# Optimization experiments

Measured on AMD Instinct MI355X. Metric: run time of the kernel, lower is better.

## Reference

```python
import jax, jax.numpy as jnp
import numpy as np
from jax.scipy.special import digamma, gammaln

B, N, H, W, D = 16, 1024, 32, 32, 256
TEMP = 0.5
KL_WEIGHT = 1e-3


def setup_inputs() -> dict:
    key = jax.random.key(0)
    k1, k2, k3 = jax.random.split(key, 3)
    logits = jax.random.normal(k1, (B, N, H, W), dtype=jnp.float32)
    # codebook initialized uniform(-1/N, 1/N) as in init_type == 'uniform'
    codebook = jax.random.uniform(k2, (N, D), dtype=jnp.float32,
                                  minval=-1.0 / N, maxval=1.0 / N)
    # uniform noise for the Gumbel-softmax rsample (channels-last layout [B,H,W,N])
    uniform_noise = jax.random.uniform(k3, (B, H, W, N), dtype=jnp.float32,
                                       minval=1e-6, maxval=1.0 - 1e-6)
    return {"logits": logits, "codebook": codebook, "uniform_noise": uniform_noise}


def reference(logits, codebook, uniform_noise):
    # convert_to_alpha: evidential mapping alpha = softplus(logits) + 1,
    # then permute(0,2,3,1) -> [B, H, W, N]
    alpha = jax.nn.softplus(jnp.transpose(logits, (0, 2, 3, 1))) + 1.0
    S = jnp.sum(alpha, axis=-1, keepdims=True)            # [B,H,W,1]
    probs = alpha / S                                      # [B,H,W,N]

    # RelaxedOneHotCategorical(temp, probs).rsample() == Gumbel-softmax
    gumbel = -jnp.log(-jnp.log(uniform_noise))
    sample = jax.nn.softmax((jnp.log(probs) + gumbel) / TEMP, axis=-1)  # [B,H,W,N]

    vector_weights = jnp.transpose(sample, (0, 3, 1, 2))   # [B,N,H,W]
    indices = jnp.argmax(vector_weights, axis=1)           # [B,H,W]

    # quantized output via codebook combine
    z_q = jnp.einsum('bnhw,nd->bdhw', vector_weights, codebook)  # [B,D,H,W]

    # KL( Dirichlet(alpha) || Dirichlet(ones(N)) ), closed form with beta=1:
    # lgamma(S) - sum lgamma(alpha) - lgamma(N) + sum (alpha-1)*(digamma(alpha)-digamma(S))
    S1 = S[..., 0]
    kl = (gammaln(S1)
          - jnp.sum(gammaln(alpha), axis=-1)
          - gammaln(jnp.float32(N))
          + jnp.sum((alpha - 1.0) * (digamma(alpha) - digamma(S)), axis=-1))
    kl_loss = KL_WEIGHT * jnp.mean(kl)

    # perplexity over soft encodings
    avg_probs = jnp.mean(sample.reshape(-1, N), axis=0)
    perplexity = jnp.exp(-jnp.sum(avg_probs * jnp.log(avg_probs + 1e-10)))

    return (z_q, kl_loss, indices, perplexity)
```

## Files before the change

kernel.cpp:

```cpp
#include <hip/hip_runtime.h>
#include <math.h>

#define NB 16
#define NN 1024
#define NH 32
#define NW 32
#define ND 256
#define NPIX (NB*NH*NW)

#define ZQ_OFF  0
#define KL_OFF  4194304
#define IDX_OFF 4194305
#define PPL_OFF 4210689

#define LGAMMA_1024F 6071.2804f
#define BS_ROW_B 2080

typedef _Float16 f16x8 __attribute__((ext_vector_type(8)));
typedef _Float16 f16x4 __attribute__((ext_vector_type(4)));
typedef float    f32x4 __attribute__((ext_vector_type(4)));

__device__ __forceinline__ float fast_rcp(float x){ return __builtin_amdgcn_rcpf(x); }

__device__ __forceinline__ void lgamma_digamma(float a, float& lg, float& dg){
    float a1 = a + 1.f, a2 = a + 2.f, z = a + 3.f;
    float t12  = a1*a2;
    float prod = a*t12;
    float rz = fast_rcp(z);
    float rp = fast_rcp(prod);
    float lz = __logf(z);
    float lp = __logf(prod);
    float rz2 = rz*rz;
    lg = (z - 0.5f)*lz - z + 0.918938533f
       + rz*(0.083333333f - 0.002777778f*rz2) - lp;
    float sr = (t12 + a*(a + a + 3.f))*rp;
    dg = lz - 0.5f*rz - rz2*(0.083333333f - 0.008333333f*rz2) - sr;
}

__device__ __forceinline__ float elem(float x, float u,
                                      float& S, float& L, float& P){
    float t  = __expf(-fabsf(x));
    float a  = fmaxf(x, 0.f) + __logf(1.f + t) + 1.f;
    float lg, dg;
    lgamma_digamma(a, lg, dg);
    S += a; L += lg; P += (a - 1.f)*dg;
    float d = 1.f - u;
    float lup = -d*(1.f + d*(0.5f + d*(0.33333333f + d*(0.25f
              + d*(0.2f + d*(0.16666667f + d*0.14285714f))))));
    float lu = (d < 0.09f) ? lup : __logf(u);
    float ar = a * fast_rcp(lu);
    return ar*ar;
}

__global__ __launch_bounds__(256) void k_tr(
    const float* __restrict__ cb, _Float16* __restrict__ cbT)
{
    const int kb = blockIdx.x, kq = blockIdx.y, d = threadIdx.x;
    _Float16 tmp[8];
#pragma unroll
    for (int i = 0; i < 8; ++i)
        tmp[i] = (_Float16)cb[(size_t)(32*kb + 8*kq + i)*ND + d];
    *(f16x8*)(cbT + (size_t)kb*8192 + (size_t)d*32 + 8*kq) = *(f16x8*)tmp;
}

__global__ __launch_bounds__(1024, 4) void k_mega(
    const float* __restrict__ logits, const float* __restrict__ noise,
    const _Float16* __restrict__ cbT, float* __restrict__ colpart,
    float* __restrict__ klpart, float* __restrict__ out)
{
    __shared__ __align__(16) char lds[16*BS_ROW_B + 6*256*4];
    char*  bsb  = lds;
    float* redS = (float*)(lds + 16*BS_ROW_B);
    float* redL = redS + 256;
    float* redP = redL + 256;
    float* redZ = redP + 256;
    float* redM = redZ + 256;
    int*   redI = (int*)(redM + 256);

    const int t    = threadIdx.x;
    const int row  = blockIdx.x >> 1;
    const int w0   = (blockIdx.x & 1) * 16;
    const int b    = row >> 5, h = row & 31;
    const int lane = t & 63;
    const int v    = t >> 6;
    const int wl   = lane & 15;
    const int j4   = (lane >> 4) & 3;
    const int p    = row*32 + w0 + wl;
    const int nq   = 4*v + j4;

    const float* lgB = logits + (size_t)b*(NN*NH*NW) + (size_t)(4*nq)*(NH*NW)
                     + (size_t)h*NW + w0 + wl;
    const float* nzB = noise  + (size_t)p*NN + 4*nq;

    float4 u4[4];
    float  xs[4][4];
    float  ev[16];
    float S = 0.f, L = 0.f, P = 0.f, Z = 0.f;
    float mx = -1.f;
    int   idx = 0;

#define CHUNK_LOAD(kk) do{                                        \
    u4[kk] = *(const float4*)(nzB + 256*(kk));                    \
    xs[kk][0] = lgB[(size_t)(256*(kk)+0)*(NH*NW)];                \
    xs[kk][1] = lgB[(size_t)(256*(kk)+1)*(NH*NW)];                \
    xs[kk][2] = lgB[(size_t)(256*(kk)+2)*(NH*NW)];                \
    xs[kk][3] = lgB[(size_t)(256*(kk)+3)*(NH*NW)]; }while(0)

#define DO_E(kk,mm,UC) do{                                        \
    float e = elem(xs[kk][mm], UC, S, L, P);                      \
    Z += e;                                                       \
    if (e > mx){ mx = e; idx = 256*(kk) + 4*nq + (mm); }          \
    ev[4*(kk)+(mm)] = e; }while(0)

    CHUNK_LOAD(0); CHUNK_LOAD(1);
    __builtin_amdgcn_sched_barrier(0);
#pragma unroll
    for (int k = 0; k < 4; ++k){
        if (k < 2){ CHUNK_LOAD(k+2); __builtin_amdgcn_sched_barrier(0); }
        DO_E(k,0,u4[k].x);
        DO_E(k,1,u4[k].y);
        DO_E(k,2,u4[k].z);
        DO_E(k,3,u4[k].w);
    }
#undef CHUNK_LOAD
#undef DO_E

#pragma unroll
    for (int mask = 16; mask < 64; mask <<= 1){
        S += __shfl_xor(S, mask);
        L += __shfl_xor(L, mask);
        P += __shfl_xor(P, mask);
        Z += __shfl_xor(Z, mask);
        float mo = __shfl_xor(mx, mask);
        int   io = __shfl_xor(idx, mask);
        bool take = (mo > mx) || (mo == mx && io < idx);
        mx  = take ? mo : mx;
        idx = take ? io : idx;
    }
    if (j4 == 0){
        redS[16*v + wl] = S;  redL[16*v + wl] = L;
        redP[16*v + wl] = P;  redZ[16*v + wl] = Z;
        redM[16*v + wl] = mx; redI[16*v + wl] = idx;
    }
    __syncthreads();

    float Zt = 0.f;
#pragma unroll
    for (int qz = 0; qz < 16; ++qz) Zt += redZ[16*qz + wl];
    const float zinv = fast_rcp(Zt);

    {
        char* brow = bsb + wl*BS_ROW_B;
        const int sw   = wl & 7;
        const int sub8 = (nq & 1) << 3;
        const int cb2  = nq >> 1;
#pragma unroll
        for (int k = 0; k < 4; ++k){
            f16x4 hv;
            hv[0] = (_Float16)(ev[4*k+0]*zinv);
            hv[1] = (_Float16)(ev[4*k+1]*zinv);
            hv[2] = (_Float16)(ev[4*k+2]*zinv);
            hv[3] = (_Float16)(ev[4*k+3]*zinv);
            *(f16x4*)(brow + (((32*k + cb2) ^ sw) << 4) + sub8) = hv;
        }
    }
    __syncthreads();

    const _Float16* aBase = cbT + (size_t)(16*v + wl)*32 + j4*8;
    const char* bRow = bsb + wl*BS_ROW_B;
    const int fsw = wl & 7;

    f32x4 acc = (f32x4)0.f;
    f16x8 ar[4];
    ar[0] = *(const f16x8*)(aBase);
    ar[1] = *(const f16x8*)(aBase + 8192);
    ar[2] = *(const f16x8*)(aBase + 2*8192);
    __builtin_amdgcn_sched_barrier(0);

#pragma unroll
    for (int kb = 0; kb < 32; ++kb){
        if (kb + 3 < 32){
            ar[(kb+3)&3] = *(const f16x8*)(aBase + (size_t)(kb+3)*8192);
            __builtin_amdgcn_sched_barrier(0);
        }
        f16x8 bf = *(const f16x8*)(bRow + ((((kb << 2) | j4) ^ fsw) << 4));
        acc = __builtin_amdgcn_mfma_f32_16x16x32_f16(ar[kb&3], bf, acc, 0, 0, 0);
    }

    float* outp = out + (size_t)b*(ND*1024) + h*32 + w0;
#pragma unroll
    for (int r = 0; r < 4; ++r){
        int d = 16*v + 4*j4 + r;
        outp[(size_t)d*1024 + wl] = acc[r];
    }

    {
        float s0 = 0.f;
#pragma unroll
        for (int r = 0; r < 16; ++r){
            const char* br = bsb + r*BS_ROW_B;
            const int sw2 = r & 7;
            s0 += (float)*(const _Float16*)(br + ((((t >> 3) ^ sw2) << 4) + 2*(t & 7)));
        }
        colpart[(size_t)blockIdx.x*NN + t] = s0;
    }

    if (t < 16){
        float Sa = 0.f, La = 0.f, Pa = 0.f, M = -1.f;
        int I = 0x7fffffff;
#pragma unroll
        for (int qz = 0; qz < 16; ++qz){
            Sa += redS[16*qz + t]; La += redL[16*qz + t]; Pa += redP[16*qz + t];
            float m = redM[16*qz + t]; int i = redI[16*qz + t];
            bool take = (m > M) || (m == M && i < I);
            M = take ? m : M; I = take ? i : I;
        }
        out[IDX_OFF + row*32 + w0 + t] = (float)I;
        float rS  = fast_rcp(Sa);
        float lnS = __logf(Sa);
        float lgS = (Sa - 0.5f)*lnS - Sa + 0.918938533f + 0.083333333f*rS;
        float dgS = lnS - 0.5f*rS;
        float kl = lgS - La - LGAMMA_1024F + (Pa - dgS*(Sa - 1024.f));
#pragma unroll
        for (int mask = 1; mask < 16; mask <<= 1) kl += __shfl_xor(kl, mask);
        if (t == 0) klpart[blockIdx.x] = kl;
    }
}

__global__ __launch_bounds__(256) void k_red(
    const float* __restrict__ colpart, float* __restrict__ colsum)
{
    __shared__ float red[8][32];
    const int nl = threadIdx.x & 31;
    const int rs = threadIdx.x >> 5;
    const int n  = blockIdx.x*32 + nl;
    const float* cp = colpart + (size_t)rs*128*NN + n;
    float s = 0.f;
#pragma unroll 8
    for (int r = 0; r < 128; ++r)
        s += cp[(size_t)r*NN];
    red[rs][nl] = s;
    __syncthreads();
    if (threadIdx.x < 32){
        float tot = 0.f;
#pragma unroll
        for (int i = 0; i < 8; ++i) tot += red[i][threadIdx.x];
        colsum[blockIdx.x*32 + threadIdx.x] = tot;
    }
}

__global__ __launch_bounds__(256) void k_final(
    const float* __restrict__ colsum, const float* __restrict__ klpart,
    float* __restrict__ out)
{
    __shared__ float red[8];
    const int tid = threadIdx.x;
    float s = 0.f, kls = 0.f;
#pragma unroll
    for (int n = tid; n < NN; n += 256){
        float avg = colsum[n] * (1.f/16384.f);
        s += avg * logf(avg + 1e-10f);
        kls += klpart[n];
    }
#pragma unroll
    for (int mask = 1; mask < 64; mask <<= 1){
        s   += __shfl_xor(s, mask);
        kls += __shfl_xor(kls, mask);
    }
    if ((tid & 63) == 0){ red[tid >> 6] = s; red[4 + (tid >> 6)] = kls; }
    __syncthreads();
    if (tid == 0){
        float tot = red[0] + red[1] + red[2] + red[3];
        float klt = red[4] + red[5] + red[6] + red[7];
        out[PPL_OFF] = expf(-tot);
        out[KL_OFF]  = 1e-3f * (klt * (1.f/16384.f));
    }
}

extern "C" void kernel_launch(void* const* d_in, const int* in_sizes, int n_in,
                              void* d_out, int out_size, void* d_ws, size_t ws_size,
                              hipStream_t stream)
{
    const float* logits = (const float*)d_in[0];
    const float* cb     = (const float*)d_in[1];
    const float* noise  = (const float*)d_in[2];
    float* out = (float*)d_out;

    float* colpart = (float*)d_ws;
    float* colsum  = colpart + (size_t)1024*NN;
    float* klpart  = colsum + NN;
    _Float16* cbT  = (_Float16*)(klpart + NN);

    k_tr   <<<dim3(32, 4), 256, 0, stream>>>(cb, cbT);
    k_mega <<<dim3(1024), 1024, 0, stream>>>(logits, noise, cbT, colpart, klpart, out);
    k_red  <<<dim3(32),    256, 0, stream>>>(colpart, colsum);
    k_final<<<1, 256, 0, stream>>>(colsum, klpart, out);
}
```

Measured before the change: 205.9 us.

## Fuse final reductions into main kernel via atomics and last-block completion

Removes the two separate reduction kernels. Column sums and KL partials are now accumulated with atomics, each on its own padded slot, and the last block to finish (tracked by a done counter) computes perplexity and KL. The per-thread accumulators are also split into two independent chains to shorten dependency latency. In exchange it adds a memset launch, 1024x1024 float atomics, and a threadfence-based completion protocol.

```diff
diff --git a/kernel.cpp b/kernel.cpp
--- a/kernel.cpp
+++ b/kernel.cpp
@@ -65,8 +65,9 @@
 
 __global__ __launch_bounds__(1024, 4) void k_mega(
     const float* __restrict__ logits, const float* __restrict__ noise,
-    const _Float16* __restrict__ cbT, float* __restrict__ colpart,
-    float* __restrict__ klpart, float* __restrict__ out)
+    const _Float16* __restrict__ cbT, float* __restrict__ colsumP,
+    float* __restrict__ klsum, unsigned int* __restrict__ done,
+    float* __restrict__ out)
 {
     __shared__ __align__(16) char lds[16*BS_ROW_B + 6*256*4];
     char*  bsb  = lds;
@@ -95,9 +96,10 @@
     float4 u4[4];
     float  xs[4][4];
     float  ev[16];
-    float S = 0.f, L = 0.f, P = 0.f, Z = 0.f;
-    float mx = -1.f;
-    int   idx = 0;
+    float Sa = 0.f, La = 0.f, Pa = 0.f, Za = 0.f;
+    float Sb = 0.f, Lb = 0.f, Pb = 0.f, Zb = 0.f;
+    float mxA = -1.f, mxB = -1.f;
+    int   idxA = 0, idxB = 0;
 
 #define CHUNK_LOAD(kk) do{                                        \
     u4[kk] = *(const float4*)(nzB + 256*(kk));                    \
@@ -106,10 +108,16 @@
     xs[kk][2] = lgB[(size_t)(256*(kk)+2)*(NH*NW)];                \
     xs[kk][3] = lgB[(size_t)(256*(kk)+3)*(NH*NW)]; }while(0)
 
-#define DO_E(kk,mm,UC) do{                                        \
-    float e = elem(xs[kk][mm], UC, S, L, P);                      \
-    Z += e;                                                       \
-    if (e > mx){ mx = e; idx = 256*(kk) + 4*nq + (mm); }          \
+#define DO_EA(kk,mm,UC) do{                                       \
+    float e = elem(xs[kk][mm], UC, Sa, La, Pa);                   \
+    Za += e;                                                      \
+    if (e > mxA){ mxA = e; idxA = 256*(kk) + 4*nq + (mm); }       \
+    ev[4*(kk)+(mm)] = e; }while(0)
+
+#define DO_EB(kk,mm,UC) do{                                       \
+    float e = elem(xs[kk][mm], UC, Sb, Lb, Pb);                   \
+    Zb += e;                                                      \
+    if (e > mxB){ mxB = e; idxB = 256*(kk) + 4*nq + (mm); }       \
     ev[4*(kk)+(mm)] = e; }while(0)
 
     CHUNK_LOAD(0); CHUNK_LOAD(1);
@@ -117,13 +125,22 @@
 #pragma unroll
     for (int k = 0; k < 4; ++k){
         if (k < 2){ CHUNK_LOAD(k+2); __builtin_amdgcn_sched_barrier(0); }
-        DO_E(k,0,u4[k].x);
-        DO_E(k,1,u4[k].y);
-        DO_E(k,2,u4[k].z);
-        DO_E(k,3,u4[k].w);
+        DO_EA(k,0,u4[k].x);
+        DO_EB(k,1,u4[k].y);
+        DO_EA(k,2,u4[k].z);
+        DO_EB(k,3,u4[k].w);
     }
 #undef CHUNK_LOAD
-#undef DO_E
+#undef DO_EA
+#undef DO_EB
+
+    float S = Sa + Sb, L = La + Lb, P = Pa + Pb, Z = Za + Zb;
+    float mx = mxA; int idx = idxA;
+    {
+        bool take = (mxB > mxA) || (mxB == mxA && idxB < idxA);
+        mx  = take ? mxB : mxA;
+        idx = take ? idxB : idxA;
+    }
 
 #pragma unroll
     for (int mask = 16; mask < 64; mask <<= 1){
@@ -202,78 +219,57 @@
             const int sw2 = r & 7;
             s0 += (float)*(const _Float16*)(br + ((((t >> 3) ^ sw2) << 4) + 2*(t & 7)));
         }
-        colpart[(size_t)blockIdx.x*NN + t] = s0;
+        atomicAdd(&colsumP[(size_t)t*32], s0);
     }
 
     if (t < 16){
-        float Sa = 0.f, La = 0.f, Pa = 0.f, M = -1.f;
+        float Sq = 0.f, Lq = 0.f, Pq = 0.f, M = -1.f;
         int I = 0x7fffffff;
 #pragma unroll
         for (int qz = 0; qz < 16; ++qz){
-            Sa += redS[16*qz + t]; La += redL[16*qz + t]; Pa += redP[16*qz + t];
+            Sq += redS[16*qz + t]; Lq += redL[16*qz + t]; Pq += redP[16*qz + t];
             float m = redM[16*qz + t]; int i = redI[16*qz + t];
             bool take = (m > M) || (m == M && i < I);
             M = take ? m : M; I = take ? i : I;
         }
         out[IDX_OFF + row*32 + w0 + t] = (float)I;
-        float rS  = fast_rcp(Sa);
-        float lnS = __logf(Sa);
-        float lgS = (Sa - 0.5f)*lnS - Sa + 0.918938533f + 0.083333333f*rS;
+        float rS  = fast_rcp(Sq);
+        float lnS = __logf(Sq);
+        float lgS = (Sq - 0.5f)*lnS - Sq + 0.918938533f + 0.083333333f*rS;
         float dgS = lnS - 0.5f*rS;
-        float kl = lgS - La - LGAMMA_1024F + (Pa - dgS*(Sa - 1024.f));
+        float kl = lgS - Lq - LGAMMA_1024F + (Pq - dgS*(Sq - 1024.f));
 #pragma unroll
         for (int mask = 1; mask < 16; mask <<= 1) kl += __shfl_xor(kl, mask);
-        if (t == 0) klpart[blockIdx.x] = kl;
-    }
-}
-
-__global__ __launch_bounds__(256) void k_red(
-    const float* __restrict__ colpart, float* __restrict__ colsum)
-{
-    __shared__ float red[8][32];
-    const int nl = threadIdx.x & 31;
-    const int rs = threadIdx.x >> 5;
-    const int n  = blockIdx.x*32 + nl;
-    const float* cp = colpart + (size_t)rs*128*NN + n;
-    float s = 0.f;
-#pragma unroll 8
-    for (int r = 0; r < 128; ++r)
-        s += cp[(size_t)r*NN];
-    red[rs][nl] = s;
-    __syncthreads();
-    if (threadIdx.x < 32){
-        float tot = 0.f;
-#pragma unroll
-        for (int i = 0; i < 8; ++i) tot += red[i][threadIdx.x];
-        colsum[blockIdx.x*32 + threadIdx.x] = tot;
-    }
-}
-
-__global__ __launch_bounds__(256) void k_final(
-    const float* __restrict__ colsum, const float* __restrict__ klpart,
-    float* __restrict__ out)
-{
-    __shared__ float red[8];
-    const int tid = threadIdx.x;
-    float s = 0.f, kls = 0.f;
-#pragma unroll
-    for (int n = tid; n < NN; n += 256){
-        float avg = colsum[n] * (1.f/16384.f);
-        s += avg * logf(avg + 1e-10f);
-        kls += klpart[n];
-    }
-#pragma unroll
-    for (int mask = 1; mask < 64; mask <<= 1){
-        s   += __shfl_xor(s, mask);
-        kls += __shfl_xor(kls, mask);
-    }
-    if ((tid & 63) == 0){ red[tid >> 6] = s; red[4 + (tid >> 6)] = kls; }
-    __syncthreads();
-    if (tid == 0){
-        float tot = red[0] + red[1] + red[2] + red[3];
-        float klt = red[4] + red[5] + red[6] + red[7];
-        out[PPL_OFF] = expf(-tot);
-        out[KL_OFF]  = 1e-3f * (klt * (1.f/16384.f));
+        if (t == 0) atomicAdd(klsum, kl);
+    }
+
+    __syncthreads();
+    int* flag = (int*)redZ;
+    if (t == 0){
+        __threadfence();
+        unsigned int old = atomicAdd(done, 1u);
+        *flag = (old == 1023u) ? 1 : 0;
+    }
+    __syncthreads();
+    if (*flag){
+        __threadfence();
+        float cv = __hip_atomic_load(&colsumP[(size_t)t*32],
+                                     __ATOMIC_RELAXED, __HIP_MEMORY_SCOPE_AGENT);
+        float avg = cv * (1.f/16384.f);
+        float s = avg * logf(avg + 1e-10f);
+#pragma unroll
+        for (int mask = 1; mask < 64; mask <<= 1) s += __shfl_xor(s, mask);
+        if (lane == 0) redL[v] = s;
+        __syncthreads();
+        if (t == 0){
+            float tot = 0.f;
+#pragma unroll
+            for (int i = 0; i < 16; ++i) tot += redL[i];
+            float kv = __hip_atomic_load(klsum, __ATOMIC_RELAXED,
+                                         __HIP_MEMORY_SCOPE_AGENT);
+            out[PPL_OFF] = expf(-tot);
+            out[KL_OFF]  = 1e-3f * (kv * (1.f/16384.f));
+        }
     }
 }
 
@@ -286,13 +282,13 @@
     const float* noise  = (const float*)d_in[2];
     float* out = (float*)d_out;
 
-    float* colpart = (float*)d_ws;
-    float* colsum  = colpart + (size_t)1024*NN;
-    float* klpart  = colsum + NN;
-    _Float16* cbT  = (_Float16*)(klpart + NN);
-
+    float* colsumP      = (float*)d_ws;
+    float* klsum        = colsumP + (size_t)1024*32;
+    unsigned int* done  = (unsigned int*)(klsum + 1);
+    _Float16* cbT       = (_Float16*)((float*)d_ws + 32772);
+
+    hipMemsetAsync(d_ws, 0, 32770u*sizeof(float), stream);
     k_tr   <<<dim3(32, 4), 256, 0, stream>>>(cb, cbT);
-    k_mega <<<dim3(1024), 1024, 0, stream>>>(logits, noise, cbT, colpart, klpart, out);
-    k_red  <<<dim3(32),    256, 0, stream>>>(colpart, colsum);
-    k_final<<<1, 256, 0, stream>>>(colsum, klpart, out);
-}
+    k_mega <<<dim3(1024), 1024, 0, stream>>>(logits, noise, cbT,
+                                             colsumP, klsum, done, out);
+}
```

Result: slower. 278.1 us (+35.0%).

## Issue all loads upfront via inline asm with staged vmcnt waits and dual accumulators

Applied to the files above, without the earlier changes.

Replaces the compiler-scheduled two-chunk prefetch with hand-written global_load asm that issues all 16 noise and logits loads at once. The loads are then consumed in four stages gated by explicit s_waitcnt vmcnt counts. Accumulators are split into two independent chains (A/B) to shorten FP dependency chains, and the launch-bounds occupancy hint drops from 4 to 2 blocks to allow more registers. This aims to maximize memory-level parallelism, at the cost of higher register pressure and fragile manual wait counts that assume no other outstanding loads.

```diff
diff --git a/kernel.cpp b/kernel.cpp
--- a/kernel.cpp
+++ b/kernel.cpp
@@ -63,7 +63,7 @@
     *(f16x8*)(cbT + (size_t)kb*8192 + (size_t)d*32 + 8*kq) = *(f16x8*)tmp;
 }
 
-__global__ __launch_bounds__(1024, 4) void k_mega(
+__global__ __launch_bounds__(1024, 2) void k_mega(
     const float* __restrict__ logits, const float* __restrict__ noise,
     const _Float16* __restrict__ cbT, float* __restrict__ colpart,
     float* __restrict__ klpart, float* __restrict__ out)
@@ -92,38 +92,77 @@
                      + (size_t)h*NW + w0 + wl;
     const float* nzB = noise  + (size_t)p*NN + 4*nq;
 
-    float4 u4[4];
-    float  xs[4][4];
-    float  ev[16];
-    float S = 0.f, L = 0.f, P = 0.f, Z = 0.f;
-    float mx = -1.f;
-    int   idx = 0;
-
-#define CHUNK_LOAD(kk) do{                                        \
-    u4[kk] = *(const float4*)(nzB + 256*(kk));                    \
-    xs[kk][0] = lgB[(size_t)(256*(kk)+0)*(NH*NW)];                \
-    xs[kk][1] = lgB[(size_t)(256*(kk)+1)*(NH*NW)];                \
-    xs[kk][2] = lgB[(size_t)(256*(kk)+2)*(NH*NW)];                \
-    xs[kk][3] = lgB[(size_t)(256*(kk)+3)*(NH*NW)]; }while(0)
-
-#define DO_E(kk,mm,UC) do{                                        \
-    float e = elem(xs[kk][mm], UC, S, L, P);                      \
-    Z += e;                                                       \
-    if (e > mx){ mx = e; idx = 256*(kk) + 4*nq + (mm); }          \
+    f32x4 u0, u1, u2, u3;
+    float x00,x01,x02,x03, x10,x11,x12,x13;
+    float x20,x21,x22,x23, x30,x31,x32,x33;
+    float ev[16];
+    float Sa = 0.f, La = 0.f, Pa = 0.f, Za = 0.f;
+    float Sb = 0.f, Lb = 0.f, Pb = 0.f, Zb = 0.f;
+    float mxA = -1.f, mxB = -1.f;
+    int   idxA = 0, idxB = 0;
+
+    asm volatile(
+        "global_load_dwordx4 %0, %4, off\n\t"
+        "global_load_dwordx4 %1, %4, off offset:1024\n\t"
+        "global_load_dwordx4 %2, %4, off offset:2048\n\t"
+        "global_load_dwordx4 %3, %4, off offset:3072"
+        : "=&v"(u0), "=&v"(u1), "=&v"(u2), "=&v"(u3)
+        : "v"(nzB));
+
+#define LG_ASM(X0,X1,X2,X3,KK) \
+    asm volatile( \
+        "global_load_dword %0, %4, off offset:-4096\n\t" \
+        "global_load_dword %1, %4, off\n\t" \
+        "global_load_dword %2, %5, off offset:-4096\n\t" \
+        "global_load_dword %3, %5, off" \
+        : "=&v"(X0), "=&v"(X1), "=&v"(X2), "=&v"(X3) \
+        : "v"(lgB + (size_t)(256*(KK))*1024 + 1024), \
+          "v"(lgB + (size_t)(256*(KK))*1024 + 3072))
+
+    LG_ASM(x00,x01,x02,x03, 0);
+    LG_ASM(x10,x11,x12,x13, 1);
+    LG_ASM(x20,x21,x22,x23, 2);
+    LG_ASM(x30,x31,x32,x33, 3);
+#undef LG_ASM
+
+#define WAITV(NSTR) do{ asm volatile("s_waitcnt vmcnt(" NSTR ")"); \
+                        __builtin_amdgcn_sched_barrier(0); }while(0)
+
+#define DO_EA(kk,mm,X,UC) do{                                     \
+    float e = elem(X, UC, Sa, La, Pa);                            \
+    Za += e;                                                      \
+    if (e > mxA){ mxA = e; idxA = 256*(kk) + 4*nq + (mm); }       \
     ev[4*(kk)+(mm)] = e; }while(0)
 
-    CHUNK_LOAD(0); CHUNK_LOAD(1);
-    __builtin_amdgcn_sched_barrier(0);
-#pragma unroll
-    for (int k = 0; k < 4; ++k){
-        if (k < 2){ CHUNK_LOAD(k+2); __builtin_amdgcn_sched_barrier(0); }
-        DO_E(k,0,u4[k].x);
-        DO_E(k,1,u4[k].y);
-        DO_E(k,2,u4[k].z);
-        DO_E(k,3,u4[k].w);
-    }
-#undef CHUNK_LOAD
-#undef DO_E
+#define DO_EB(kk,mm,X,UC) do{                                     \
+    float e = elem(X, UC, Sb, Lb, Pb);                            \
+    Zb += e;                                                      \
+    if (e > mxB){ mxB = e; idxB = 256*(kk) + 4*nq + (mm); }       \
+    ev[4*(kk)+(mm)] = e; }while(0)
+
+    WAITV("12");
+    DO_EA(0,0,x00,u0[0]); DO_EB(0,1,x01,u0[1]);
+    DO_EA(0,2,x02,u0[2]); DO_EB(0,3,x03,u0[3]);
+    WAITV("8");
+    DO_EA(1,0,x10,u1[0]); DO_EB(1,1,x11,u1[1]);
+    DO_EA(1,2,x12,u1[2]); DO_EB(1,3,x13,u1[3]);
+    WAITV("4");
+    DO_EA(2,0,x20,u2[0]); DO_EB(2,1,x21,u2[1]);
+    DO_EA(2,2,x22,u2[2]); DO_EB(2,3,x23,u2[3]);
+    WAITV("0");
+    DO_EA(3,0,x30,u3[0]); DO_EB(3,1,x31,u3[1]);
+    DO_EA(3,2,x32,u3[2]); DO_EB(3,3,x33,u3[3]);
+#undef WAITV
+#undef DO_EA
+#undef DO_EB
+
+    float S = Sa + Sb, L = La + Lb, P = Pa + Pb, Z = Za + Zb;
+    float mx; int idx;
+    {
+        bool take = (mxB > mxA) || (mxB == mxA && idxB < idxA);
+        mx  = take ? mxB : mxA;
+        idx = take ? idxB : idxA;
+    }
 
 #pragma unroll
     for (int mask = 16; mask < 64; mask <<= 1){
@@ -206,21 +245,21 @@
     }
 
     if (t < 16){
-        float Sa = 0.f, La = 0.f, Pa = 0.f, M = -1.f;
+        float Sq = 0.f, Lq = 0.f, Pq = 0.f, M = -1.f;
         int I = 0x7fffffff;
 #pragma unroll
         for (int qz = 0; qz < 16; ++qz){
-            Sa += redS[16*qz + t]; La += redL[16*qz + t]; Pa += redP[16*qz + t];
+            Sq += redS[16*qz + t]; Lq += redL[16*qz + t]; Pq += redP[16*qz + t];
             float m = redM[16*qz + t]; int i = redI[16*qz + t];
             bool take = (m > M) || (m == M && i < I);
             M = take ? m : M; I = take ? i : I;
         }
         out[IDX_OFF + row*32 + w0 + t] = (float)I;
-        float rS  = fast_rcp(Sa);
-        float lnS = __logf(Sa);
-        float lgS = (Sa - 0.5f)*lnS - Sa + 0.918938533f + 0.083333333f*rS;
+        float rS  = fast_rcp(Sq);
+        float lnS = __logf(Sq);
+        float lgS = (Sq - 0.5f)*lnS - Sq + 0.918938533f + 0.083333333f*rS;
         float dgS = lnS - 0.5f*rS;
-        float kl = lgS - La - LGAMMA_1024F + (Pa - dgS*(Sa - 1024.f));
+        float kl = lgS - Lq - LGAMMA_1024F + (Pq - dgS*(Sq - 1024.f));
 #pragma unroll
         for (int mask = 1; mask < 16; mask <<= 1) kl += __shfl_xor(kl, mask);
         if (t == 0) klpart[blockIdx.x] = kl;
```

Measured after the change: 204.5 us. No clear change (-0.7%).
